# Optimization experiments

Hardware: AMD Instinct MI355X
Metric: run time of the kernel (lower is better)

Reference implementation:

```python
import jax, jax.numpy as jnp
import numpy as np

N, E = 50000, 800000
IN_F, HID, OUT, HEADS = 128, 64, 128, 4
NEG_SLOPE = 0.2


def setup_inputs() -> dict:
    key = jax.random.key(0)
    ks = jax.random.split(key, 10)
    s = 0.05
    return {
        "x": jax.random.normal(ks[0], (N, IN_F), dtype=jnp.float32),
        "edge_index": jax.random.randint(ks[1], (2, E), 0, N, dtype=jnp.int64),
        "W1": jax.random.normal(ks[2], (IN_F, HEADS * HID), dtype=jnp.float32) * s,
        "att_src1": jax.random.normal(ks[3], (HEADS, HID), dtype=jnp.float32) * s,
        "att_dst1": jax.random.normal(ks[4], (HEADS, HID), dtype=jnp.float32) * s,
        "b1": jnp.zeros((HEADS * HID,), dtype=jnp.float32),
        "W2": jax.random.normal(ks[5], (HEADS * HID, OUT), dtype=jnp.float32) * s,
        "att_src2": jax.random.normal(ks[6], (1, OUT), dtype=jnp.float32) * s,
        "att_dst2": jax.random.normal(ks[7], (1, OUT), dtype=jnp.float32) * s,
        "b2": jnp.zeros((OUT,), dtype=jnp.float32),
    }


def _gat_layer(x, W, a_src, a_dst, b, src, dst, heads, out_c):
    n = x.shape[0]
    h = (x @ W).reshape(n, heads, out_c)              # [N, H, C]
    alpha_s = jnp.einsum("nhc,hc->nh", h, a_src)       # [N, H]
    alpha_d = jnp.einsum("nhc,hc->nh", h, a_dst)
    e = jax.nn.leaky_relu(alpha_s[src] + alpha_d[dst], NEG_SLOPE)  # [E, H]
    # scatter-softmax over edges grouped by destination node
    m = jax.ops.segment_max(e, dst, num_segments=n)
    ex = jnp.exp(e - m[dst])
    denom = jax.ops.segment_sum(ex, dst, num_segments=n)
    alpha = ex / denom[dst]                            # [E, H]
    out = jax.ops.segment_sum(alpha[:, :, None] * h[src], dst, num_segments=n)
    return out.reshape(n, heads * out_c) + b


def reference(x, edge_index, W1, att_src1, att_dst1, b1, W2, att_src2, att_dst2, b2):
    n = x.shape[0]
    loop = jnp.arange(n, dtype=edge_index.dtype)       # PyG add_self_loops=True
    src = jnp.concatenate([edge_index[0], loop])
    dst = jnp.concatenate([edge_index[1], loop])
    h = _gat_layer(x, W1, att_src1, att_dst1, b1, src, dst, HEADS, HID)
    h = jax.nn.elu(h)
    out = _gat_layer(h, W2, att_src2, att_dst2, b2, src, dst, 1, OUT)
    return out
```

## Files before the change

### kernel.cpp

```cpp
#include <hip/hip_runtime.h>
#include <hip/hip_bf16.h>

#define NEG_SLOPE 0.2f

typedef short bf16x8 __attribute__((ext_vector_type(8)));
typedef float f32x4 __attribute__((ext_vector_type(4)));
typedef float f32x2 __attribute__((ext_vector_type(2)));

__device__ __forceinline__ unsigned short f2bf(float f) {
    unsigned int x = __float_as_uint(f);
    unsigned int lsb = (x >> 16) & 1u;
    x += 0x7fffu + lsb;
    return (unsigned short)(x >> 16);
}
__device__ __forceinline__ f32x2 upk(unsigned int u) {
    f32x2 r;
    r.x = __uint_as_float(u << 16);
    r.y = __uint_as_float(u & 0xffff0000u);
    return r;
}
__device__ __forceinline__ unsigned short f2h(float f) {
    _Float16 h = (_Float16)f;
    return *(unsigned short*)&h;
}
__device__ __forceinline__ float h2f(unsigned short u) {
    _Float16 h = *(_Float16*)&u;
    return (float)h;
}

__global__ void cast_w_both(const float* __restrict__ W1, const float* __restrict__ W2,
                            unsigned short* __restrict__ wt1, unsigned short* __restrict__ wt2) {
    int idx = blockIdx.x * 256 + threadIdx.x;
    if (idx < 128 * 256) {
        int k = idx >> 8, n = idx & 255;
        wt1[(size_t)n * 128 + k] = f2bf(W1[idx]);
    } else {
        int j = idx - 128 * 256;
        int k = j >> 7, n = j & 127;
        wt2[(size_t)n * 256 + k] = f2bf(W2[j]);
    }
}

__global__ void degree_kernel(const int* __restrict__ ei, int E, int N,
                              int* __restrict__ deg, int* __restrict__ idx) {
    int e = blockIdx.x * blockDim.x + threadIdx.x;
    int EA = E + N;
    if (e >= EA) return;
    int dst = (e < E) ? ei[E + e] : (e - E);
    idx[e] = atomicAdd(&deg[dst], 1);
}

__global__ void scan_local(const int* __restrict__ deg, int* __restrict__ offs,
                           int* __restrict__ bsum, int N) {
    __shared__ int wsum[16];
    int tid = threadIdx.x;
    int lane = tid & 63;
    int wave = tid >> 6;
    int i = blockIdx.x * 1024 + tid;
    int v = (i < N) ? deg[i] : 0;
    int x = v;
    #pragma unroll
    for (int off = 1; off < 64; off <<= 1) {
        int t = __shfl_up(x, off);
        if (lane >= off) x += t;
    }
    if (lane == 63) wsum[wave] = x;
    __syncthreads();
    if (wave == 0 && lane < 16) {
        int w = wsum[lane];
        #pragma unroll
        for (int off = 1; off < 16; off <<= 1) {
            int t = __shfl_up(w, off);
            if (lane >= off) w += t;
        }
        wsum[lane] = w;
    }
    __syncthreads();
    int wexcl = (wave > 0) ? wsum[wave - 1] : 0;
    if (i <= N) offs[i] = wexcl + x - v;
    if (tid == 0) bsum[blockIdx.x] = wsum[15];
}

__global__ void scan_add(int* __restrict__ offs, const int* __restrict__ bsum,
                         int N, int nb) {
    int lane = threadIdx.x & 63;
    int v = (lane < nb) ? bsum[lane] : 0;
    int x = v;
    #pragma unroll
    for (int off = 1; off < 64; off <<= 1) {
        int t = __shfl_up(x, off);
        if (lane >= off) x += t;
    }
    int excl = __shfl(x - v, blockIdx.x);
    int i = blockIdx.x * 1024 + threadIdx.x;
    if (i <= N) offs[i] += excl;
}

__global__ void scatter_kernel(const int* __restrict__ ei, int E, int N,
                               const int* __restrict__ offs, const int* __restrict__ idx,
                               const float* __restrict__ as1, const float* __restrict__ ad1,
                               int* __restrict__ colb, uint2* __restrict__ p1) {
    int e = blockIdx.x * blockDim.x + threadIdx.x;
    int EA = E + N;
    if (e >= EA) return;
    int s, d;
    if (e < E) { s = ei[e]; d = ei[E + e]; }
    else       { s = d = e - E; }
    int pos = offs[d] + idx[e];
    colb[pos] = s << 9;
    float4 av = *(const float4*)(as1 + s * 4);
    float4 dv = *(const float4*)(ad1 + d * 4);
    float e0 = av.x + dv.x, e1 = av.y + dv.y, e2 = av.z + dv.z, e3 = av.w + dv.w;
    e0 = (e0 > 0.f) ? e0 : NEG_SLOPE * e0;
    e1 = (e1 > 0.f) ? e1 : NEG_SLOPE * e1;
    e2 = (e2 > 0.f) ? e2 : NEG_SLOPE * e2;
    e3 = (e3 > 0.f) ? e3 : NEG_SLOPE * e3;
    uint2 q;
    q.x = (unsigned int)f2h(__expf(e0)) | ((unsigned int)f2h(__expf(e1)) << 16);
    q.y = (unsigned int)f2h(__expf(e2)) | ((unsigned int)f2h(__expf(e3)) << 16);
    p1[pos] = q;
}

__global__ void gemm1_mfma(const float* __restrict__ A,
                           const unsigned short* __restrict__ Wt,
                           const float* __restrict__ att_s, const float* __restrict__ att_d,
                           unsigned short* __restrict__ hb,
                           float* __restrict__ as, float* __restrict__ ad, int M) {
    int wave = threadIdx.x >> 6;
    int lane = threadIdx.x & 63;
    int quad = lane >> 4;
    int l16 = lane & 15;
    int m0 = blockIdx.x * 64 + wave * 16;
    int rowc = min(m0 + l16, M - 1);
    bf16x8 a[4];
    const float* ap = A + (size_t)rowc * 128 + quad * 8;
    #pragma unroll
    for (int kc = 0; kc < 4; ++kc) {
        float4 f0 = *(const float4*)(ap + kc * 32);
        float4 f1 = *(const float4*)(ap + kc * 32 + 4);
        bf16x8 v;
        v[0] = (short)f2bf(f0.x); v[1] = (short)f2bf(f0.y);
        v[2] = (short)f2bf(f0.z); v[3] = (short)f2bf(f0.w);
        v[4] = (short)f2bf(f1.x); v[5] = (short)f2bf(f1.y);
        v[6] = (short)f2bf(f1.z); v[7] = (short)f2bf(f1.w);
        a[kc] = v;
    }
    f32x4 acc[16];
    #pragma unroll
    for (int nt = 0; nt < 16; ++nt) {
        f32x4 c = {0.f, 0.f, 0.f, 0.f};
        const unsigned short* bp = Wt + (size_t)(nt * 16 + l16) * 128 + quad * 8;
        #pragma unroll
        for (int kc = 0; kc < 4; ++kc) {
            bf16x8 b = *(const bf16x8*)(bp + kc * 32);
            c = __builtin_amdgcn_mfma_f32_16x16x32_bf16(a[kc], b, c, 0, 0, 0);
        }
        acc[nt] = c;
    }
    float asv[16], adv[16];
    #pragma unroll
    for (int nt = 0; nt < 16; ++nt) {
        asv[nt] = att_s[nt * 16 + l16];
        adv[nt] = att_d[nt * 16 + l16];
    }
    int srow0 = m0 + quad * 4;
    #pragma unroll
    for (int r = 0; r < 4; ++r) {
        int srow = srow0 + r;
        bool ok = srow < M;
        if (ok) {
            #pragma unroll
            for (int nt = 0; nt < 16; ++nt)
                hb[(size_t)srow * 256 + nt * 16 + l16] = f2bf(acc[nt][r]);
        }
        #pragma unroll
        for (int h = 0; h < 4; ++h) {
            float ps = acc[4 * h][r] * asv[4 * h] + acc[4 * h + 1][r] * asv[4 * h + 1]
                     + acc[4 * h + 2][r] * asv[4 * h + 2] + acc[4 * h + 3][r] * asv[4 * h + 3];
            float pd = acc[4 * h][r] * adv[4 * h] + acc[4 * h + 1][r] * adv[4 * h + 1]
                     + acc[4 * h + 2][r] * adv[4 * h + 2] + acc[4 * h + 3][r] * adv[4 * h + 3];
            #pragma unroll
            for (int off = 1; off < 16; off <<= 1) {
                ps += __shfl_xor(ps, off);
                pd += __shfl_xor(pd, off);
            }
            if (ok && l16 == 0) {
                as[srow * 4 + h] = ps;
                ad[srow * 4 + h] = pd;
            }
        }
    }
}

__global__ void gemm2_mfma(const unsigned short* __restrict__ Ab,
                           const unsigned short* __restrict__ Wt,
                           const float* __restrict__ att_s, const float* __restrict__ att_d,
                           unsigned short* __restrict__ hb,
                           float* __restrict__ as, float* __restrict__ ad, int M) {
    int wave = threadIdx.x >> 6;
    int lane = threadIdx.x & 63;
    int quad = lane >> 4;
    int l16 = lane & 15;
    int m0 = blockIdx.x * 64 + wave * 16;
    int rowc = min(m0 + l16, M - 1);
    bf16x8 a[8];
    const unsigned short* ap = Ab + (size_t)rowc * 256 + quad * 8;
    #pragma unroll
    for (int kc = 0; kc < 8; ++kc) a[kc] = *(const bf16x8*)(ap + kc * 32);
    f32x4 acc[8];
    #pragma unroll
    for (int nt = 0; nt < 8; ++nt) {
        f32x4 c = {0.f, 0.f, 0.f, 0.f};
        const unsigned short* bp = Wt + (size_t)(nt * 16 + l16) * 256 + quad * 8;
        #pragma unroll
        for (int kc = 0; kc < 8; ++kc) {
            bf16x8 b = *(const bf16x8*)(bp + kc * 32);
            c = __builtin_amdgcn_mfma_f32_16x16x32_bf16(a[kc], b, c, 0, 0, 0);
        }
        acc[nt] = c;
    }
    float asv[8], adv[8];
    #pragma unroll
    for (int nt = 0; nt < 8; ++nt) {
        asv[nt] = att_s[nt * 16 + l16];
        adv[nt] = att_d[nt * 16 + l16];
    }
    int srow0 = m0 + quad * 4;
    #pragma unroll
    for (int r = 0; r < 4; ++r) {
        int srow = srow0 + r;
        bool ok = srow < M;
        if (ok) {
            #pragma unroll
            for (int nt = 0; nt < 8; ++nt)
                hb[(size_t)srow * 128 + nt * 16 + l16] = f2bf(acc[nt][r]);
        }
        float ps = 0.f, pd = 0.f;
        #pragma unroll
        for (int nt = 0; nt < 8; ++nt) {
            ps = fmaf(acc[nt][r], asv[nt], ps);
            pd = fmaf(acc[nt][r], adv[nt], pd);
        }
        #pragma unroll
        for (int off = 1; off < 16; off <<= 1) {
            ps += __shfl_xor(ps, off);
            pd += __shfl_xor(pd, off);
        }
        if (ok && l16 == 0) { as[srow] = ps; ad[srow] = pd; }
    }
}

__global__ void agg1_kernel(const unsigned short* __restrict__ hb,
                            const int* __restrict__ colb, const uint2* __restrict__ p1,
                            const int* __restrict__ offs,
                            const float* __restrict__ b1,
                            unsigned short* __restrict__ out, int N) {
    int node = blockIdx.x * 4 + (threadIdx.x >> 6);
    if (node >= N) return;
    int lane = threadIdx.x & 63;
    int half = lane >> 5;
    int sub  = lane & 31;
    int head = sub >> 3;
    int c0b = sub * 16;
    const char* hpc = (const char*)hb;
    int beg = offs[node], end = offs[node + 1];
    float d = 0.f;
    f32x2 acc[4] = {};
    int j = beg + half;
    for (; j + 6 < end; j += 8) {
        int o0 = colb[j] + c0b;
        int o1 = colb[j + 2] + c0b;
        int o2 = colb[j + 4] + c0b;
        int o3 = colb[j + 6] + c0b;
        uint2 q0 = p1[j];
        uint2 q1 = p1[j + 2];
        uint2 q2 = p1[j + 4];
        uint2 q3 = p1[j + 6];
        uint4 g0 = *(const uint4*)(hpc + o0);
        uint4 g1 = *(const uint4*)(hpc + o1);
        uint4 g2 = *(const uint4*)(hpc + o2);
        uint4 g3 = *(const uint4*)(hpc + o3);
        unsigned int u0 = (head & 2) ? q0.y : q0.x;
        unsigned int u1 = (head & 2) ? q1.y : q1.x;
        unsigned int u2 = (head & 2) ? q2.y : q2.x;
        unsigned int u3 = (head & 2) ? q3.y : q3.x;
        float p0 = h2f((unsigned short)((head & 1) ? (u0 >> 16) : (u0 & 0xffff)));
        float p1v = h2f((unsigned short)((head & 1) ? (u1 >> 16) : (u1 & 0xffff)));
        float p2 = h2f((unsigned short)((head & 1) ? (u2 >> 16) : (u2 & 0xffff)));
        float p3 = h2f((unsigned short)((head & 1) ? (u3 >> 16) : (u3 & 0xffff)));
        d += (p0 + p1v) + (p2 + p3);
        const unsigned int* w0 = (const unsigned int*)&g0;
        const unsigned int* w1 = (const unsigned int*)&g1;
        const unsigned int* w2 = (const unsigned int*)&g2;
        const unsigned int* w3 = (const unsigned int*)&g3;
        f32x2 v0 = {p0, p0}, v1 = {p1v, p1v}, v2 = {p2, p2}, v3 = {p3, p3};
        #pragma unroll
        for (int i = 0; i < 4; ++i) {
            acc[i] = __builtin_elementwise_fma(v0, upk(w0[i]), acc[i]);
            acc[i] = __builtin_elementwise_fma(v1, upk(w1[i]), acc[i]);
            acc[i] = __builtin_elementwise_fma(v2, upk(w2[i]), acc[i]);
            acc[i] = __builtin_elementwise_fma(v3, upk(w3[i]), acc[i]);
        }
    }
    for (; j < end; j += 2) {
        int o = colb[j] + c0b;
        uint2 q = p1[j];
        uint4 g = *(const uint4*)(hpc + o);
        unsigned int u = (head & 2) ? q.y : q.x;
        float p = h2f((unsigned short)((head & 1) ? (u >> 16) : (u & 0xffff)));
        d += p;
        const unsigned int* w = (const unsigned int*)&g;
        f32x2 v = {p, p};
        #pragma unroll
        for (int i = 0; i < 4; ++i)
            acc[i] = __builtin_elementwise_fma(v, upk(w[i]), acc[i]);
    }
    d += __shfl_xor(d, 32);
    #pragma unroll
    for (int i = 0; i < 4; ++i) {
        acc[i].x += __shfl_xor(acc[i].x, 32);
        acc[i].y += __shfl_xor(acc[i].y, 32);
    }
    if (half == 0) {
        float inv = 1.f / d;
        int c0 = sub * 8;
        float4 bb0 = *(const float4*)(b1 + c0);
        float4 bb1 = *(const float4*)(b1 + c0 + 4);
        float av[8] = {acc[0].x, acc[0].y, acc[1].x, acc[1].y,
                       acc[2].x, acc[2].y, acc[3].x, acc[3].y};
        float bb[8] = {bb0.x, bb0.y, bb0.z, bb0.w, bb1.x, bb1.y, bb1.z, bb1.w};
        unsigned short o[8];
        #pragma unroll
        for (int i = 0; i < 8; ++i) {
            float v = av[i] * inv + bb[i];
            v = (v > 0.f) ? v : (__expf(v) - 1.f);
            o[i] = f2bf(v);
        }
        ushort4 q0 = {o[0], o[1], o[2], o[3]};
        ushort4 q1 = {o[4], o[5], o[6], o[7]};
        *(ushort4*)(out + (size_t)node * 256 + c0) = q0;
        *(ushort4*)(out + (size_t)node * 256 + c0 + 4) = q1;
    }
}

__global__ void agg2_kernel(const unsigned short* __restrict__ hb,
                            const float* __restrict__ as,
                            const float* __restrict__ ad,
                            const int* __restrict__ offs, const int* __restrict__ colb,
                            const float* __restrict__ b2,
                            float* __restrict__ out, int N) {
    int node = blockIdx.x * 4 + (threadIdx.x >> 6);
    if (node >= N) return;
    int lane = threadIdx.x & 63;
    int q   = lane >> 4;
    int sub = lane & 15;
    int c0b = sub * 16;
    const char* hpc = (const char*)hb;
    float adv = ad[node];
    int beg = offs[node], end = offs[node + 1];
    float d = 0.f;
    f32x2 acc[4] = {};
    int j = beg + q;
    for (; j + 4 < end; j += 8) {
        int cb0 = colb[j];
        int cb1 = colb[j + 4];
        uint4 g0 = *(const uint4*)(hpc + (cb0 >> 1) + c0b);
        uint4 g1 = *(const uint4*)(hpc + (cb1 >> 1) + c0b);
        float e0 = as[cb0 >> 9] + adv;
        float e1 = as[cb1 >> 9] + adv;
        e0 = (e0 > 0.f) ? e0 : NEG_SLOPE * e0;
        e1 = (e1 > 0.f) ? e1 : NEG_SLOPE * e1;
        float p0 = __expf(e0), p1 = __expf(e1);
        d += p0 + p1;
        const unsigned int* w0 = (const unsigned int*)&g0;
        const unsigned int* w1 = (const unsigned int*)&g1;
        f32x2 v0 = {p0, p0}, v1 = {p1, p1};
        #pragma unroll
        for (int i = 0; i < 4; ++i) {
            acc[i] = __builtin_elementwise_fma(v0, upk(w0[i]), acc[i]);
            acc[i] = __builtin_elementwise_fma(v1, upk(w1[i]), acc[i]);
        }
    }
    for (; j < end; j += 4) {
        int cb = colb[j];
        uint4 g = *(const uint4*)(hpc + (cb >> 1) + c0b);
        float e = as[cb >> 9] + adv;
        e = (e > 0.f) ? e : NEG_SLOPE * e;
        float p = __expf(e);
        d += p;
        const unsigned int* w = (const unsigned int*)&g;
        f32x2 v = {p, p};
        #pragma unroll
        for (int i = 0; i < 4; ++i)
            acc[i] = __builtin_elementwise_fma(v, upk(w[i]), acc[i]);
    }
    d += __shfl_xor(d, 16);
    d += __shfl_xor(d, 32);
    #pragma unroll
    for (int i = 0; i < 4; ++i) {
        acc[i].x += __shfl_xor(acc[i].x, 16);
        acc[i].x += __shfl_xor(acc[i].x, 32);
        acc[i].y += __shfl_xor(acc[i].y, 16);
        acc[i].y += __shfl_xor(acc[i].y, 32);
    }
    if (lane < 16) {
        float inv = 1.f / d;
        int c0 = sub * 8;
        float4 bb0 = *(const float4*)(b2 + c0);
        float4 bb1 = *(const float4*)(b2 + c0 + 4);
        float av[8] = {acc[0].x, acc[0].y, acc[1].x, acc[1].y,
                       acc[2].x, acc[2].y, acc[3].x, acc[3].y};
        float bb[8] = {bb0.x, bb0.y, bb0.z, bb0.w, bb1.x, bb1.y, bb1.z, bb1.w};
        *(float4*)(out + (size_t)node * 128 + c0) =
            make_float4(av[0] * inv + bb[0], av[1] * inv + bb[1],
                        av[2] * inv + bb[2], av[3] * inv + bb[3]);
        *(float4*)(out + (size_t)node * 128 + c0 + 4) =
            make_float4(av[4] * inv + bb[4], av[5] * inv + bb[5],
                        av[6] * inv + bb[6], av[7] * inv + bb[7]);
    }
}


extern "C" void kernel_launch(void* const* d_in, const int* in_sizes, int n_in,
                              void* d_out, int out_size, void* d_ws, size_t ws_size,
                              hipStream_t stream) {
    const float* x    = (const float*)d_in[0];
    const int*   ei   = (const int*)d_in[1];
    const float* W1   = (const float*)d_in[2];
    const float* at_s1 = (const float*)d_in[3];
    const float* at_d1 = (const float*)d_in[4];
    const float* b1   = (const float*)d_in[5];
    const float* W2   = (const float*)d_in[6];
    const float* at_s2 = (const float*)d_in[7];
    const float* at_d2 = (const float*)d_in[8];
    const float* b2   = (const float*)d_in[9];
    float* out = (float*)d_out;

    const int N  = in_sizes[0] / 128;
    const int E  = in_sizes[1] / 2;
    const int EA = E + N;

    char* ws = (char*)d_ws;
    size_t off = 0;
    auto alloc = [&](size_t bytes) -> void* {
        void* p = ws + off;
        off += (bytes + 255) & ~(size_t)255;
        return p;
    };
    unsigned short* wt1  = (unsigned short*)alloc((size_t)256 * 128 * 2);
    unsigned short* wt2  = (unsigned short*)alloc((size_t)128 * 256 * 2);
    unsigned short* h1b  = (unsigned short*)alloc((size_t)N * 256 * 2);
    unsigned short* h1ab = (unsigned short*)alloc((size_t)N * 256 * 2);
    unsigned short* h2b  = (unsigned short*)alloc((size_t)N * 128 * 2);
    float* as1 = (float*)alloc((size_t)N * 4 * 4);
    float* ad1 = (float*)alloc((size_t)N * 4 * 4);
    float* as2 = (float*)alloc((size_t)N * 4);
    float* ad2 = (float*)alloc((size_t)N * 4);
    int* deg  = (int*)alloc((size_t)N * 4);
    int* idx  = (int*)alloc((size_t)EA * 4);
    int* offs = (int*)alloc((size_t)(N + 1) * 4);
    int* bsum = (int*)alloc((size_t)1024 * 4);
    int* colb = (int*)alloc((size_t)EA * 4);
    uint2* p1 = (uint2*)alloc((size_t)EA * 8);

    const int nb = (N + 1 + 1023) / 1024;

    hipMemsetAsync(deg, 0, (size_t)N * 4, stream);
    cast_w_both<<<(2 * 128 * 256 + 255) / 256, 256, 0, stream>>>(W1, W2, wt1, wt2);
    degree_kernel<<<(EA + 255) / 256, 256, 0, stream>>>(ei, E, N, deg, idx);
    scan_local<<<nb, 1024, 0, stream>>>(deg, offs, bsum, N);
    scan_add<<<nb, 1024, 0, stream>>>(offs, bsum, N, nb);

    gemm1_mfma<<<(N + 63) / 64, 256, 0, stream>>>(x, wt1, at_s1, at_d1, h1b, as1, ad1, N);
    scatter_kernel<<<(EA + 255) / 256, 256, 0, stream>>>(ei, E, N, offs, idx, as1, ad1,
                                                         colb, p1);
    agg1_kernel<<<(N + 3) / 4, 256, 0, stream>>>(h1b, colb, p1, offs, b1, h1ab, N);

    gemm2_mfma<<<(N + 63) / 64, 256, 0, stream>>>(h1ab, wt2, at_s2, at_d2, h2b, as2, ad2, N);
    agg2_kernel<<<(N + 3) / 4, 256, 0, stream>>>(h2b, as2, ad2, offs, colb, b2, out, N);
}
```

Baseline: 330.5 us.

## Double rows per wave in GEMMs and precompute layer-2 edge weights in CSR order

Both MFMA GEMM kernels now process 32 rows per wave (two 16-row tiles) so each loaded weight fragment feeds two MFMAs, halving B-operand loads per output row and the number of blocks. A new edge kernel computes the layer-2 attention exponentials once per edge and writes them in CSR order. agg2 then reads these weights contiguously instead of gathering as2 by source and computing exp in its inner loop. This adds a kernel launch, an extra edge-sized buffer and more register pressure in the GEMMs, which may lower occupancy.

```diff
diff --git a/kernel.cpp b/kernel.cpp
--- a/kernel.cpp
+++ b/kernel.cpp
@@ -121,6 +121,22 @@
     p1[pos] = q;
 }
 
+__global__ void edgew2_kernel(const int* __restrict__ ei, int E, int N,
+                              const int* __restrict__ offs, const int* __restrict__ idx,
+                              const float* __restrict__ as2, const float* __restrict__ ad2,
+                              float* __restrict__ p2) {
+    int e = blockIdx.x * blockDim.x + threadIdx.x;
+    int EA = E + N;
+    if (e >= EA) return;
+    int s, d;
+    if (e < E) { s = ei[e]; d = ei[E + e]; }
+    else       { s = d = e - E; }
+    int pos = offs[d] + idx[e];
+    float ev = as2[s] + ad2[d];
+    ev = (ev > 0.f) ? ev : NEG_SLOPE * ev;
+    p2[pos] = __expf(ev);
+}
+
 __global__ void gemm1_mfma(const float* __restrict__ A,
                            const unsigned short* __restrict__ Wt,
                            const float* __restrict__ att_s, const float* __restrict__ att_d,
@@ -130,32 +146,42 @@
     int lane = threadIdx.x & 63;
     int quad = lane >> 4;
     int l16 = lane & 15;
-    int m0 = blockIdx.x * 64 + wave * 16;
-    int rowc = min(m0 + l16, M - 1);
-    bf16x8 a[4];
-    const float* ap = A + (size_t)rowc * 128 + quad * 8;
+    int m0 = blockIdx.x * 128 + wave * 32;
+    int r0c = min(m0 + l16, M - 1);
+    int r1c = min(m0 + 16 + l16, M - 1);
+    bf16x8 a0[4], a1[4];
     #pragma unroll
     for (int kc = 0; kc < 4; ++kc) {
-        float4 f0 = *(const float4*)(ap + kc * 32);
-        float4 f1 = *(const float4*)(ap + kc * 32 + 4);
-        bf16x8 v;
-        v[0] = (short)f2bf(f0.x); v[1] = (short)f2bf(f0.y);
-        v[2] = (short)f2bf(f0.z); v[3] = (short)f2bf(f0.w);
-        v[4] = (short)f2bf(f1.x); v[5] = (short)f2bf(f1.y);
-        v[6] = (short)f2bf(f1.z); v[7] = (short)f2bf(f1.w);
-        a[kc] = v;
-    }
-    f32x4 acc[16];
+        const float* p0 = A + (size_t)r0c * 128 + quad * 8 + kc * 32;
+        const float* p1 = A + (size_t)r1c * 128 + quad * 8 + kc * 32;
+        float4 f0 = *(const float4*)(p0);
+        float4 f1 = *(const float4*)(p0 + 4);
+        float4 g0 = *(const float4*)(p1);
+        float4 g1 = *(const float4*)(p1 + 4);
+        bf16x8 v0, v1;
+        v0[0] = (short)f2bf(f0.x); v0[1] = (short)f2bf(f0.y);
+        v0[2] = (short)f2bf(f0.z); v0[3] = (short)f2bf(f0.w);
+        v0[4] = (short)f2bf(f1.x); v0[5] = (short)f2bf(f1.y);
+        v0[6] = (short)f2bf(f1.z); v0[7] = (short)f2bf(f1.w);
+        v1[0] = (short)f2bf(g0.x); v1[1] = (short)f2bf(g0.y);
+        v1[2] = (short)f2bf(g0.z); v1[3] = (short)f2bf(g0.w);
+        v1[4] = (short)f2bf(g1.x); v1[5] = (short)f2bf(g1.y);
+        v1[6] = (short)f2bf(g1.z); v1[7] = (short)f2bf(g1.w);
+        a0[kc] = v0; a1[kc] = v1;
+    }
+    f32x4 acc0[16], acc1[16];
     #pragma unroll
     for (int nt = 0; nt < 16; ++nt) {
-        f32x4 c = {0.f, 0.f, 0.f, 0.f};
+        f32x4 c0 = {0.f, 0.f, 0.f, 0.f};
+        f32x4 c1 = {0.f, 0.f, 0.f, 0.f};
         const unsigned short* bp = Wt + (size_t)(nt * 16 + l16) * 128 + quad * 8;
         #pragma unroll
         for (int kc = 0; kc < 4; ++kc) {
             bf16x8 b = *(const bf16x8*)(bp + kc * 32);
-            c = __builtin_amdgcn_mfma_f32_16x16x32_bf16(a[kc], b, c, 0, 0, 0);
-        }
-        acc[nt] = c;
+            c0 = __builtin_amdgcn_mfma_f32_16x16x32_bf16(a0[kc], b, c0, 0, 0, 0);
+            c1 = __builtin_amdgcn_mfma_f32_16x16x32_bf16(a1[kc], b, c1, 0, 0, 0);
+        }
+        acc0[nt] = c0; acc1[nt] = c1;
     }
     float asv[16], adv[16];
     #pragma unroll
@@ -163,30 +189,34 @@
         asv[nt] = att_s[nt * 16 + l16];
         adv[nt] = att_d[nt * 16 + l16];
     }
-    int srow0 = m0 + quad * 4;
-    #pragma unroll
-    for (int r = 0; r < 4; ++r) {
-        int srow = srow0 + r;
-        bool ok = srow < M;
-        if (ok) {
+    #pragma unroll
+    for (int g = 0; g < 2; ++g) {
+        f32x4* acc = g ? acc1 : acc0;
+        int srow0 = m0 + g * 16 + quad * 4;
+        #pragma unroll
+        for (int r = 0; r < 4; ++r) {
+            int srow = srow0 + r;
+            bool ok = srow < M;
+            if (ok) {
+                #pragma unroll
+                for (int nt = 0; nt < 16; ++nt)
+                    hb[(size_t)srow * 256 + nt * 16 + l16] = f2bf(acc[nt][r]);
+            }
             #pragma unroll
-            for (int nt = 0; nt < 16; ++nt)
-                hb[(size_t)srow * 256 + nt * 16 + l16] = f2bf(acc[nt][r]);
-        }
-        #pragma unroll
-        for (int h = 0; h < 4; ++h) {
-            float ps = acc[4 * h][r] * asv[4 * h] + acc[4 * h + 1][r] * asv[4 * h + 1]
-                     + acc[4 * h + 2][r] * asv[4 * h + 2] + acc[4 * h + 3][r] * asv[4 * h + 3];
-            float pd = acc[4 * h][r] * adv[4 * h] + acc[4 * h + 1][r] * adv[4 * h + 1]
-                     + acc[4 * h + 2][r] * adv[4 * h + 2] + acc[4 * h + 3][r] * adv[4 * h + 3];
-            #pragma unroll
-            for (int off = 1; off < 16; off <<= 1) {
-                ps += __shfl_xor(ps, off);
-                pd += __shfl_xor(pd, off);
-            }
-            if (ok && l16 == 0) {
-                as[srow * 4 + h] = ps;
-                ad[srow * 4 + h] = pd;
+            for (int h = 0; h < 4; ++h) {
+                float ps = acc[4 * h][r] * asv[4 * h] + acc[4 * h + 1][r] * asv[4 * h + 1]
+                         + acc[4 * h + 2][r] * asv[4 * h + 2] + acc[4 * h + 3][r] * asv[4 * h + 3];
+                float pd = acc[4 * h][r] * adv[4 * h] + acc[4 * h + 1][r] * adv[4 * h + 1]
+                         + acc[4 * h + 2][r] * adv[4 * h + 2] + acc[4 * h + 3][r] * adv[4 * h + 3];
+                #pragma unroll
+                for (int off = 1; off < 16; off <<= 1) {
+                    ps += __shfl_xor(ps, off);
+                    pd += __shfl_xor(pd, off);
+                }
+                if (ok && l16 == 0) {
+                    as[srow * 4 + h] = ps;
+                    ad[srow * 4 + h] = pd;
+                }
             }
         }
     }
@@ -201,23 +231,30 @@
     int lane = threadIdx.x & 63;
     int quad = lane >> 4;
     int l16 = lane & 15;
-    int m0 = blockIdx.x * 64 + wave * 16;
-    int rowc = min(m0 + l16, M - 1);
-    bf16x8 a[8];
-    const unsigned short* ap = Ab + (size_t)rowc * 256 + quad * 8;
-    #pragma unroll
-    for (int kc = 0; kc < 8; ++kc) a[kc] = *(const bf16x8*)(ap + kc * 32);
-    f32x4 acc[8];
+    int m0 = blockIdx.x * 128 + wave * 32;
+    int r0c = min(m0 + l16, M - 1);
+    int r1c = min(m0 + 16 + l16, M - 1);
+    bf16x8 a0[8], a1[8];
+    const unsigned short* ap0 = Ab + (size_t)r0c * 256 + quad * 8;
+    const unsigned short* ap1 = Ab + (size_t)r1c * 256 + quad * 8;
+    #pragma unroll
+    for (int kc = 0; kc < 8; ++kc) {
+        a0[kc] = *(const bf16x8*)(ap0 + kc * 32);
+        a1[kc] = *(const bf16x8*)(ap1 + kc * 32);
+    }
+    f32x4 acc0[8], acc1[8];
     #pragma unroll
     for (int nt = 0; nt < 8; ++nt) {
-        f32x4 c = {0.f, 0.f, 0.f, 0.f};
+        f32x4 c0 = {0.f, 0.f, 0.f, 0.f};
+        f32x4 c1 = {0.f, 0.f, 0.f, 0.f};
         const unsigned short* bp = Wt + (size_t)(nt * 16 + l16) * 256 + quad * 8;
         #pragma unroll
         for (int kc = 0; kc < 8; ++kc) {
             bf16x8 b = *(const bf16x8*)(bp + kc * 32);
-            c = __builtin_amdgcn_mfma_f32_16x16x32_bf16(a[kc], b, c, 0, 0, 0);
-        }
-        acc[nt] = c;
+            c0 = __builtin_amdgcn_mfma_f32_16x16x32_bf16(a0[kc], b, c0, 0, 0, 0);
+            c1 = __builtin_amdgcn_mfma_f32_16x16x32_bf16(a1[kc], b, c1, 0, 0, 0);
+        }
+        acc0[nt] = c0; acc1[nt] = c1;
     }
     float asv[8], adv[8];
     #pragma unroll
@@ -225,28 +262,32 @@
         asv[nt] = att_s[nt * 16 + l16];
         adv[nt] = att_d[nt * 16 + l16];
     }
-    int srow0 = m0 + quad * 4;
-    #pragma unroll
-    for (int r = 0; r < 4; ++r) {
-        int srow = srow0 + r;
-        bool ok = srow < M;
-        if (ok) {
+    #pragma unroll
+    for (int g = 0; g < 2; ++g) {
+        f32x4* acc = g ? acc1 : acc0;
+        int srow0 = m0 + g * 16 + quad * 4;
+        #pragma unroll
+        for (int r = 0; r < 4; ++r) {
+            int srow = srow0 + r;
+            bool ok = srow < M;
+            if (ok) {
+                #pragma unroll
+                for (int nt = 0; nt < 8; ++nt)
+                    hb[(size_t)srow * 128 + nt * 16 + l16] = f2bf(acc[nt][r]);
+            }
+            float ps = 0.f, pd = 0.f;
             #pragma unroll
-            for (int nt = 0; nt < 8; ++nt)
-                hb[(size_t)srow * 128 + nt * 16 + l16] = f2bf(acc[nt][r]);
-        }
-        float ps = 0.f, pd = 0.f;
-        #pragma unroll
-        for (int nt = 0; nt < 8; ++nt) {
-            ps = fmaf(acc[nt][r], asv[nt], ps);
-            pd = fmaf(acc[nt][r], adv[nt], pd);
-        }
-        #pragma unroll
-        for (int off = 1; off < 16; off <<= 1) {
-            ps += __shfl_xor(ps, off);
-            pd += __shfl_xor(pd, off);
-        }
-        if (ok && l16 == 0) { as[srow] = ps; ad[srow] = pd; }
+            for (int nt = 0; nt < 8; ++nt) {
+                ps = fmaf(acc[nt][r], asv[nt], ps);
+                pd = fmaf(acc[nt][r], adv[nt], pd);
+            }
+            #pragma unroll
+            for (int off = 1; off < 16; off <<= 1) {
+                ps += __shfl_xor(ps, off);
+                pd += __shfl_xor(pd, off);
+            }
+            if (ok && l16 == 0) { as[srow] = ps; ad[srow] = pd; }
+        }
     }
 }
 
@@ -344,8 +385,7 @@
 }
 
 __global__ void agg2_kernel(const unsigned short* __restrict__ hb,
-                            const float* __restrict__ as,
-                            const float* __restrict__ ad,
+                            const float* __restrict__ p2,
                             const int* __restrict__ offs, const int* __restrict__ colb,
                             const float* __restrict__ b2,
                             float* __restrict__ out, int N) {
@@ -356,7 +396,6 @@
     int sub = lane & 15;
     int c0b = sub * 16;
     const char* hpc = (const char*)hb;
-    float adv = ad[node];
     int beg = offs[node], end = offs[node + 1];
     float d = 0.f;
     f32x2 acc[4] = {};
@@ -364,13 +403,10 @@
     for (; j + 4 < end; j += 8) {
         int cb0 = colb[j];
         int cb1 = colb[j + 4];
+        float p0 = p2[j];
+        float p1 = p2[j + 4];
         uint4 g0 = *(const uint4*)(hpc + (cb0 >> 1) + c0b);
         uint4 g1 = *(const uint4*)(hpc + (cb1 >> 1) + c0b);
-        float e0 = as[cb0 >> 9] + adv;
-        float e1 = as[cb1 >> 9] + adv;
-        e0 = (e0 > 0.f) ? e0 : NEG_SLOPE * e0;
-        e1 = (e1 > 0.f) ? e1 : NEG_SLOPE * e1;
-        float p0 = __expf(e0), p1 = __expf(e1);
         d += p0 + p1;
         const unsigned int* w0 = (const unsigned int*)&g0;
         const unsigned int* w1 = (const unsigned int*)&g1;
@@ -383,10 +419,8 @@
     }
     for (; j < end; j += 4) {
         int cb = colb[j];
+        float p = p2[j];
         uint4 g = *(const uint4*)(hpc + (cb >> 1) + c0b);
-        float e = as[cb >> 9] + adv;
-        e = (e > 0.f) ? e : NEG_SLOPE * e;
-        float p = __expf(e);
         d += p;
         const unsigned int* w = (const unsigned int*)&g;
         f32x2 v = {p, p};
@@ -462,6 +496,7 @@
     int* bsum = (int*)alloc((size_t)1024 * 4);
     int* colb = (int*)alloc((size_t)EA * 4);
     uint2* p1 = (uint2*)alloc((size_t)EA * 8);
+    float* p2 = (float*)alloc((size_t)EA * 4);
 
     const int nb = (N + 1 + 1023) / 1024;
 
@@ -471,11 +506,12 @@
     scan_local<<<nb, 1024, 0, stream>>>(deg, offs, bsum, N);
     scan_add<<<nb, 1024, 0, stream>>>(offs, bsum, N, nb);
 
-    gemm1_mfma<<<(N + 63) / 64, 256, 0, stream>>>(x, wt1, at_s1, at_d1, h1b, as1, ad1, N);
+    gemm1_mfma<<<(N + 127) / 128, 256, 0, stream>>>(x, wt1, at_s1, at_d1, h1b, as1, ad1, N);
     scatter_kernel<<<(EA + 255) / 256, 256, 0, stream>>>(ei, E, N, offs, idx, as1, ad1,
                                                          colb, p1);
     agg1_kernel<<<(N + 3) / 4, 256, 0, stream>>>(h1b, colb, p1, offs, b1, h1ab, N);
 
-    gemm2_mfma<<<(N + 63) / 64, 256, 0, stream>>>(h1ab, wt2, at_s2, at_d2, h2b, as2, ad2, N);
-    agg2_kernel<<<(N + 3) / 4, 256, 0, stream>>>(h2b, as2, ad2, offs, colb, b2, out, N);
-}
+    gemm2_mfma<<<(N + 127) / 128, 256, 0, stream>>>(h1ab, wt2, at_s2, at_d2, h2b, as2, ad2, N);
+    edgew2_kernel<<<(EA + 255) / 256, 256, 0, stream>>>(ei, E, N, offs, idx, as2, ad2, p2);
+    agg2_kernel<<<(N + 3) / 4, 256, 0, stream>>>(h2b, p2, offs, colb, b2, out, N);
+}
```

New measurement: 357.7 us. 1.08x slower.

## Permute hidden layout for vectorized GEMM1 stores and precompute layer-2 edge weights

Applied to the files above, without the earlier changes.

The layer-1 hidden features are stored in a permuted column order, so each lane writes 16 contiguous bf16 values as two 16-byte stores instead of 16 scattered 2-byte stores. W2's cast is permuted to match, and the agg1 head/bias indexing is rearranged so each lane handles two heads. A new edge kernel precomputes the layer-2 exp attention weights in CSR order, so agg2 no longer does a random as2 lookup and exp per edge. This adds an extra launch and an EA-sized float buffer.

```diff
diff --git a/kernel.cpp b/kernel.cpp
--- a/kernel.cpp
+++ b/kernel.cpp
@@ -36,8 +36,10 @@
         wt1[(size_t)n * 128 + k] = f2bf(W1[idx]);
     } else {
         int j = idx - 128 * 256;
-        int k = j >> 7, n = j & 127;
-        wt2[(size_t)n * 256 + k] = f2bf(W2[j]);
+        int n = j >> 8;
+        int p = j & 255;
+        int c = (p & 15) * 16 + (p >> 4);
+        wt2[(size_t)n * 256 + p] = f2bf(W2[(size_t)c * 128 + n]);
     }
 }
 
@@ -121,6 +123,22 @@
     p1[pos] = q;
 }
 
+__global__ void edgew2_kernel(const int* __restrict__ ei, int E, int N,
+                              const int* __restrict__ offs, const int* __restrict__ idx,
+                              const float* __restrict__ as2, const float* __restrict__ ad2,
+                              float* __restrict__ p2) {
+    int e = blockIdx.x * blockDim.x + threadIdx.x;
+    int EA = E + N;
+    if (e >= EA) return;
+    int s, d;
+    if (e < E) { s = ei[e]; d = ei[E + e]; }
+    else       { s = d = e - E; }
+    int pos = offs[d] + idx[e];
+    float ev = as2[s] + ad2[d];
+    ev = (ev > 0.f) ? ev : NEG_SLOPE * ev;
+    p2[pos] = __expf(ev);
+}
+
 __global__ void gemm1_mfma(const float* __restrict__ A,
                            const unsigned short* __restrict__ Wt,
                            const float* __restrict__ att_s, const float* __restrict__ att_d,
@@ -169,9 +187,15 @@
         int srow = srow0 + r;
         bool ok = srow < M;
         if (ok) {
+            unsigned int pk[8];
             #pragma unroll
-            for (int nt = 0; nt < 16; ++nt)
-                hb[(size_t)srow * 256 + nt * 16 + l16] = f2bf(acc[nt][r]);
+            for (int i = 0; i < 8; ++i)
+                pk[i] = (unsigned int)f2bf(acc[2 * i][r]) |
+                        ((unsigned int)f2bf(acc[2 * i + 1][r]) << 16);
+            uint4 lo = {pk[0], pk[1], pk[2], pk[3]};
+            uint4 hi = {pk[4], pk[5], pk[6], pk[7]};
+            *(uint4*)(hb + (size_t)srow * 256 + l16 * 16) = lo;
+            *(uint4*)(hb + (size_t)srow * 256 + l16 * 16 + 8) = hi;
         }
         #pragma unroll
         for (int h = 0; h < 4; ++h) {
@@ -260,11 +284,10 @@
     int lane = threadIdx.x & 63;
     int half = lane >> 5;
     int sub  = lane & 31;
-    int head = sub >> 3;
     int c0b = sub * 16;
     const char* hpc = (const char*)hb;
     int beg = offs[node], end = offs[node + 1];
-    float d = 0.f;
+    float dL = 0.f, dH = 0.f;
     f32x2 acc[4] = {};
     int j = beg + half;
     for (; j + 6 < end; j += 8) {
@@ -280,72 +303,85 @@
         uint4 g1 = *(const uint4*)(hpc + o1);
         uint4 g2 = *(const uint4*)(hpc + o2);
         uint4 g3 = *(const uint4*)(hpc + o3);
-        unsigned int u0 = (head & 2) ? q0.y : q0.x;
-        unsigned int u1 = (head & 2) ? q1.y : q1.x;
-        unsigned int u2 = (head & 2) ? q2.y : q2.x;
-        unsigned int u3 = (head & 2) ? q3.y : q3.x;
-        float p0 = h2f((unsigned short)((head & 1) ? (u0 >> 16) : (u0 & 0xffff)));
-        float p1v = h2f((unsigned short)((head & 1) ? (u1 >> 16) : (u1 & 0xffff)));
-        float p2 = h2f((unsigned short)((head & 1) ? (u2 >> 16) : (u2 & 0xffff)));
-        float p3 = h2f((unsigned short)((head & 1) ? (u3 >> 16) : (u3 & 0xffff)));
-        d += (p0 + p1v) + (p2 + p3);
+        unsigned int u0 = (sub & 1) ? q0.y : q0.x;
+        unsigned int u1 = (sub & 1) ? q1.y : q1.x;
+        unsigned int u2 = (sub & 1) ? q2.y : q2.x;
+        unsigned int u3 = (sub & 1) ? q3.y : q3.x;
+        float pL0 = h2f((unsigned short)(u0 & 0xffff)), pH0 = h2f((unsigned short)(u0 >> 16));
+        float pL1 = h2f((unsigned short)(u1 & 0xffff)), pH1 = h2f((unsigned short)(u1 >> 16));
+        float pL2 = h2f((unsigned short)(u2 & 0xffff)), pH2 = h2f((unsigned short)(u2 >> 16));
+        float pL3 = h2f((unsigned short)(u3 & 0xffff)), pH3 = h2f((unsigned short)(u3 >> 16));
+        dL += (pL0 + pL1) + (pL2 + pL3);
+        dH += (pH0 + pH1) + (pH2 + pH3);
         const unsigned int* w0 = (const unsigned int*)&g0;
         const unsigned int* w1 = (const unsigned int*)&g1;
         const unsigned int* w2 = (const unsigned int*)&g2;
         const unsigned int* w3 = (const unsigned int*)&g3;
-        f32x2 v0 = {p0, p0}, v1 = {p1v, p1v}, v2 = {p2, p2}, v3 = {p3, p3};
-        #pragma unroll
-        for (int i = 0; i < 4; ++i) {
-            acc[i] = __builtin_elementwise_fma(v0, upk(w0[i]), acc[i]);
-            acc[i] = __builtin_elementwise_fma(v1, upk(w1[i]), acc[i]);
-            acc[i] = __builtin_elementwise_fma(v2, upk(w2[i]), acc[i]);
-            acc[i] = __builtin_elementwise_fma(v3, upk(w3[i]), acc[i]);
+        f32x2 vL0 = {pL0, pL0}, vH0 = {pH0, pH0};
+        f32x2 vL1 = {pL1, pL1}, vH1 = {pH1, pH1};
+        f32x2 vL2 = {pL2, pL2}, vH2 = {pH2, pH2};
+        f32x2 vL3 = {pL3, pL3}, vH3 = {pH3, pH3};
+        #pragma unroll
+        for (int i = 0; i < 2; ++i) {
+            acc[i] = __builtin_elementwise_fma(vL0, upk(w0[i]), acc[i]);
+            acc[i] = __builtin_elementwise_fma(vL1, upk(w1[i]), acc[i]);
+            acc[i] = __builtin_elementwise_fma(vL2, upk(w2[i]), acc[i]);
+            acc[i] = __builtin_elementwise_fma(vL3, upk(w3[i]), acc[i]);
+            acc[i + 2] = __builtin_elementwise_fma(vH0, upk(w0[i + 2]), acc[i + 2]);
+            acc[i + 2] = __builtin_elementwise_fma(vH1, upk(w1[i + 2]), acc[i + 2]);
+            acc[i + 2] = __builtin_elementwise_fma(vH2, upk(w2[i + 2]), acc[i + 2]);
+            acc[i + 2] = __builtin_elementwise_fma(vH3, upk(w3[i + 2]), acc[i + 2]);
         }
     }
     for (; j < end; j += 2) {
         int o = colb[j] + c0b;
         uint2 q = p1[j];
         uint4 g = *(const uint4*)(hpc + o);
-        unsigned int u = (head & 2) ? q.y : q.x;
-        float p = h2f((unsigned short)((head & 1) ? (u >> 16) : (u & 0xffff)));
-        d += p;
+        unsigned int u = (sub & 1) ? q.y : q.x;
+        float pL = h2f((unsigned short)(u & 0xffff));
+        float pH = h2f((unsigned short)(u >> 16));
+        dL += pL;
+        dH += pH;
         const unsigned int* w = (const unsigned int*)&g;
-        f32x2 v = {p, p};
-        #pragma unroll
-        for (int i = 0; i < 4; ++i)
-            acc[i] = __builtin_elementwise_fma(v, upk(w[i]), acc[i]);
-    }
-    d += __shfl_xor(d, 32);
+        f32x2 vL = {pL, pL}, vH = {pH, pH};
+        #pragma unroll
+        for (int i = 0; i < 2; ++i) {
+            acc[i] = __builtin_elementwise_fma(vL, upk(w[i]), acc[i]);
+            acc[i + 2] = __builtin_elementwise_fma(vH, upk(w[i + 2]), acc[i + 2]);
+        }
+    }
+    dL += __shfl_xor(dL, 32);
+    dH += __shfl_xor(dH, 32);
     #pragma unroll
     for (int i = 0; i < 4; ++i) {
         acc[i].x += __shfl_xor(acc[i].x, 32);
         acc[i].y += __shfl_xor(acc[i].y, 32);
     }
     if (half == 0) {
-        float inv = 1.f / d;
-        int c0 = sub * 8;
-        float4 bb0 = *(const float4*)(b1 + c0);
-        float4 bb1 = *(const float4*)(b1 + c0 + 4);
+        float invL = 1.f / dL;
+        float invH = 1.f / dH;
         float av[8] = {acc[0].x, acc[0].y, acc[1].x, acc[1].y,
                        acc[2].x, acc[2].y, acc[3].x, acc[3].y};
-        float bb[8] = {bb0.x, bb0.y, bb0.z, bb0.w, bb1.x, bb1.y, bb1.z, bb1.w};
         unsigned short o[8];
+        int base16 = sub >> 1;
+        int lo16 = 8 * (sub & 1);
         #pragma unroll
         for (int i = 0; i < 8; ++i) {
-            float v = av[i] * inv + bb[i];
+            float inv = (i < 4) ? invL : invH;
+            float bbv = b1[(lo16 + i) * 16 + base16];
+            float v = av[i] * inv + bbv;
             v = (v > 0.f) ? v : (__expf(v) - 1.f);
             o[i] = f2bf(v);
         }
         ushort4 q0 = {o[0], o[1], o[2], o[3]};
         ushort4 q1 = {o[4], o[5], o[6], o[7]};
-        *(ushort4*)(out + (size_t)node * 256 + c0) = q0;
-        *(ushort4*)(out + (size_t)node * 256 + c0 + 4) = q1;
+        *(ushort4*)(out + (size_t)node * 256 + sub * 8) = q0;
+        *(ushort4*)(out + (size_t)node * 256 + sub * 8 + 4) = q1;
     }
 }
 
 __global__ void agg2_kernel(const unsigned short* __restrict__ hb,
-                            const float* __restrict__ as,
-                            const float* __restrict__ ad,
+                            const float* __restrict__ p2,
                             const int* __restrict__ offs, const int* __restrict__ colb,
                             const float* __restrict__ b2,
                             float* __restrict__ out, int N) {
@@ -356,7 +392,6 @@
     int sub = lane & 15;
     int c0b = sub * 16;
     const char* hpc = (const char*)hb;
-    float adv = ad[node];
     int beg = offs[node], end = offs[node + 1];
     float d = 0.f;
     f32x2 acc[4] = {};
@@ -364,13 +399,10 @@
     for (; j + 4 < end; j += 8) {
         int cb0 = colb[j];
         int cb1 = colb[j + 4];
+        float p0 = p2[j];
+        float p1 = p2[j + 4];
         uint4 g0 = *(const uint4*)(hpc + (cb0 >> 1) + c0b);
         uint4 g1 = *(const uint4*)(hpc + (cb1 >> 1) + c0b);
-        float e0 = as[cb0 >> 9] + adv;
-        float e1 = as[cb1 >> 9] + adv;
-        e0 = (e0 > 0.f) ? e0 : NEG_SLOPE * e0;
-        e1 = (e1 > 0.f) ? e1 : NEG_SLOPE * e1;
-        float p0 = __expf(e0), p1 = __expf(e1);
         d += p0 + p1;
         const unsigned int* w0 = (const unsigned int*)&g0;
         const unsigned int* w1 = (const unsigned int*)&g1;
@@ -383,10 +415,8 @@
     }
     for (; j < end; j += 4) {
         int cb = colb[j];
+        float p = p2[j];
         uint4 g = *(const uint4*)(hpc + (cb >> 1) + c0b);
-        float e = as[cb >> 9] + adv;
-        e = (e > 0.f) ? e : NEG_SLOPE * e;
-        float p = __expf(e);
         d += p;
         const unsigned int* w = (const unsigned int*)&g;
         f32x2 v = {p, p};
@@ -462,6 +492,7 @@
     int* bsum = (int*)alloc((size_t)1024 * 4);
     int* colb = (int*)alloc((size_t)EA * 4);
     uint2* p1 = (uint2*)alloc((size_t)EA * 8);
+    float* p2 = (float*)alloc((size_t)EA * 4);
 
     const int nb = (N + 1 + 1023) / 1024;
 
@@ -477,5 +508,6 @@
     agg1_kernel<<<(N + 3) / 4, 256, 0, stream>>>(h1b, colb, p1, offs, b1, h1ab, N);
 
     gemm2_mfma<<<(N + 63) / 64, 256, 0, stream>>>(h1ab, wt2, at_s2, at_d2, h2b, as2, ad2, N);
-    agg2_kernel<<<(N + 3) / 4, 256, 0, stream>>>(h2b, as2, ad2, offs, colb, b2, out, N);
-}
+    edgew2_kernel<<<(EA + 255) / 256, 256, 0, stream>>>(ei, E, N, offs, idx, as2, ad2, p2);
+    agg2_kernel<<<(N + 3) / 4, 256, 0, stream>>>(h2b, p2, offs, colb, b2, out, N);
+}
```

Result: slower. 348.8 us (+5.5%).
